# Performance work log

Measured on AMD Instinct MI355X. Metric: run time of the kernel, lower is better.

## Reference

```python
import jax, jax.numpy as jnp
import numpy as np

TEMPERATURE = 0.2
EPS = 1e-10

def setup_inputs() -> dict:
    key = jax.random.key(0)
    x = jax.random.normal(key, (8, 1024, 64, 64), dtype=jnp.float32)
    return {"x": x}

def reference(x):
    B, C, H, W = x.shape
    xf = x.reshape(B, C, H * W)                      # [B, C, HW]
    dot = jnp.einsum('bcn,bdn->bcd', xf, xf) / TEMPERATURE  # [B, C, C]
    logits = jax.nn.softmax(dot, axis=-1)
    diag = jnp.diagonal(logits, axis1=-2, axis2=-1)  # [B, C]
    loss = -jnp.log(diag + EPS)
    return jnp.mean(loss)
```

## Files before the change

### kernel.cpp

```cpp
#include <hip/hip_runtime.h>
#include <hip/hip_bf16.h>

#define BATCH 8
#define CCH 1024
#define NHW 4096
#define SCALE 5.0f
#define ROWS (BATCH * CCH)

typedef unsigned char u8;
typedef unsigned int u32;
typedef __attribute__((ext_vector_type(4))) float float4v;
typedef __attribute__((ext_vector_type(4))) u32 uint4v;

#define VMW(N) asm volatile("s_waitcnt vmcnt(" #N ")" ::: "memory")

__device__ __forceinline__ void async_load16(const void* gsrc, void* ldst) {
    __builtin_amdgcn_global_load_lds(
        (__attribute__((address_space(1))) void*)gsrc,
        (__attribute__((address_space(3))) void*)ldst,
        16, 0, 0);
}

__device__ __forceinline__ u32 pk4_fp8(float a, float b, float c, float d) {
    u32 v = __builtin_amdgcn_cvt_pk_fp8_f32(a, b, 0, false);
    v = __builtin_amdgcn_cvt_pk_fp8_f32(c, d, v, true);
    return v;
}

__device__ __forceinline__ float ssq4_fp8(u32 q) {
    float d0 = __builtin_amdgcn_cvt_f32_fp8(q, 0);
    float d1 = __builtin_amdgcn_cvt_f32_fp8(q, 1);
    float d2 = __builtin_amdgcn_cvt_f32_fp8(q, 2);
    float d3 = __builtin_amdgcn_cvt_f32_fp8(q, 3);
    return d0 * d0 + d1 * d1 + d2 * d2 + d3 * d3;
}

template <bool CONVERT>
__global__ __launch_bounds__(256) void prep_kernel(const float* __restrict__ x,
                                                   u8* __restrict__ xq,
                                                   float* __restrict__ diag,
                                                   float* __restrict__ l_acc,
                                                   u32* __restrict__ counter) {
    const int row = blockIdx.x;
    const int tid = threadIdx.x;
    const float* src = x + (size_t)row * NHW;
    float ssum = 0.f;
#pragma unroll
    for (int p = 0; p < 4; ++p) {
        const int idx = p * 1024 + tid * 4;
        float4 v = *(const float4*)(src + idx);
        const u32 q = pk4_fp8(v.x, v.y, v.z, v.w);
        ssum += ssq4_fp8(q);
        if (CONVERT) *(u32*)(xq + (size_t)row * NHW + idx) = q;
    }
#pragma unroll
    for (int m = 1; m < 64; m <<= 1) ssum += __shfl_xor(ssum, m);
    __shared__ float red[4];
    if ((tid & 63) == 0) red[tid >> 6] = ssum;
    __syncthreads();
    if (tid == 0) {
        diag[row] = (red[0] + red[1] + red[2] + red[3]) * SCALE;
        l_acc[row] = 0.f;
        if (row == 0) *counter = 0;
    }
}

template <bool QSRC>
__global__ __launch_bounds__(256) void gram_kernel(const u8* __restrict__ Xq,
                                                   const float* __restrict__ Xf,
                                                   const float* __restrict__ diag,
                                                   float* __restrict__ l_acc,
                                                   float* __restrict__ num,
                                                   u32* __restrict__ counter,
                                                   float* __restrict__ out) {
    __shared__ __align__(16) u8 As[2][16384];
    __shared__ __align__(16) u8 Bs[2][8192];

    const int bid = blockIdx.x;
    const int b = bid & 7;
    const int t = bid >> 3;

    int bi = 0;
#pragma unroll
    for (int i = 7; i >= 1; --i) {
        if (t >= i * (17 - i)) { bi = i; break; }
    }
    const int bj2 = 2 * bi + (t - bi * (17 - bi));
    const bool aliasB = (bj2 == 2 * bi) || (bj2 == 2 * bi + 1);

    const int tid  = threadIdx.x;
    const int lane = tid & 63;
    const int w    = tid >> 6;
    const int wm   = w >> 1;
    const int wn   = w & 1;

    const int st_r  = lane >> 3;
    const int st_kc = (lane & 7) ^ st_r;

    const u8*    pA  = nullptr; const u8*    pB  = nullptr;
    const float* pAf = nullptr; const float* pBf = nullptr;
    if (QSRC) {
        const u8* baseX = Xq + (size_t)b * CCH * NHW;
        pA = baseX + (size_t)(bi * 128 + w * 32 + st_r) * NHW + st_kc * 16;
        pB = baseX + (size_t)(bj2 * 64 + w * 16 + st_r) * NHW + st_kc * 16;
    } else {
        const float* baseXf = Xf + (size_t)b * CCH * NHW;
        pAf = baseXf + (size_t)(bi * 128 + w * 32 + st_r) * NHW + st_kc * 16;
        pBf = baseXf + (size_t)(bj2 * 64 + w * 16 + st_r) * NHW + st_kc * 16;
    }

    float4v acc[4][2] = {};

    auto stage = [&](int buf, int K0) {
        if (QSRC) {
#pragma unroll
            for (int t8 = 0; t8 < 4; ++t8)
                async_load16(pA + (size_t)(t8 * 8) * NHW + K0,
                             As[buf] + (size_t)(w * 32 + t8 * 8) * 128);
            if (!aliasB) {
#pragma unroll
                for (int t8 = 0; t8 < 2; ++t8)
                    async_load16(pB + (size_t)(t8 * 8) * NHW + K0,
                                 Bs[buf] + (size_t)(w * 16 + t8 * 8) * 128);
            }
        } else {
#pragma unroll
            for (int t8 = 0; t8 < 4; ++t8) {
                const float* s = pAf + (size_t)(t8 * 8) * NHW + K0;
                float4 f0 = *(const float4*)(s);
                float4 f1 = *(const float4*)(s + 4);
                float4 f2 = *(const float4*)(s + 8);
                float4 f3 = *(const float4*)(s + 12);
                uint4v d;
                d.x = pk4_fp8(f0.x, f0.y, f0.z, f0.w);
                d.y = pk4_fp8(f1.x, f1.y, f1.z, f1.w);
                d.z = pk4_fp8(f2.x, f2.y, f2.z, f2.w);
                d.w = pk4_fp8(f3.x, f3.y, f3.z, f3.w);
                *(uint4v*)(As[buf] + (size_t)(w * 32 + t8 * 8 + st_r) * 128 + (lane & 7) * 16) = d;
            }
            if (!aliasB) {
#pragma unroll
                for (int t8 = 0; t8 < 2; ++t8) {
                    const float* s = pBf + (size_t)(t8 * 8) * NHW + K0;
                    float4 f0 = *(const float4*)(s);
                    float4 f1 = *(const float4*)(s + 4);
                    float4 f2 = *(const float4*)(s + 8);
                    float4 f3 = *(const float4*)(s + 12);
                    uint4v d;
                    d.x = pk4_fp8(f0.x, f0.y, f0.z, f0.w);
                    d.y = pk4_fp8(f1.x, f1.y, f1.z, f1.w);
                    d.z = pk4_fp8(f2.x, f2.y, f2.z, f2.w);
                    d.w = pk4_fp8(f3.x, f3.y, f3.z, f3.w);
                    *(uint4v*)(Bs[buf] + (size_t)(w * 16 + t8 * 8 + st_r) * 128 + (lane & 7) * 16) = d;
                }
            }
        }
    };

    stage(0, 0);
    if (!QSRC) __syncthreads();

    const int q  = lane >> 4;
    const int rl = lane & 15;

    for (int i = 0; i < NHW / 128; ++i) {
        const int cur = i & 1;
        const int K0n = (i + 1) * 128;
        const bool more = (K0n < NHW);
        if (more) stage(cur ^ 1, K0n);

        if (QSRC) {
            if (more) {
                if (aliasB) VMW(4); else VMW(6);
            } else {
                VMW(0);
            }
            __builtin_amdgcn_s_barrier();
            __builtin_amdgcn_sched_barrier(0);
        } else {
            __syncthreads();
        }

        const u8* Ab = As[cur];
        const u8* Bb = aliasB ? (Ab + (size_t)(bj2 - 2 * bi) * 64 * 128) : Bs[cur];
#pragma unroll
        for (int s = 0; s < 4; ++s) {
            const int cbase = 2 * s + (q >> 1);
            const int boff  = (int)((cbase ^ (rl & 7)) * 16 + (q & 1) * 8);
            long af[4], bf[2];
#pragma unroll
            for (int mt = 0; mt < 4; ++mt)
                af[mt] = *(const long*)(Ab + (size_t)(wm * 64 + mt * 16 + rl) * 128 + boff);
#pragma unroll
            for (int nt = 0; nt < 2; ++nt)
                bf[nt] = *(const long*)(Bb + (size_t)(wn * 32 + nt * 16 + rl) * 128 + boff);
#pragma unroll
            for (int mt = 0; mt < 4; ++mt)
#pragma unroll
                for (int nt = 0; nt < 2; ++nt)
                    acc[mt][nt] = __builtin_amdgcn_mfma_f32_16x16x32_fp8_fp8(af[mt], bf[nt], acc[mt][nt], 0, 0, 0);
        }

        if (QSRC) {
            __builtin_amdgcn_sched_barrier(0);
            __builtin_amdgcn_s_barrier();
        } else {
            __syncthreads();
        }
    }

    const int cl = lane & 15;
    const int rowbase = bi * 128 + wm * 64;
    const int colbase = bj2 * 64 + wn * 32;
    const float* dgb = diag + b * CCH;
    float* lb = l_acc + b * CCH;

#pragma unroll
    for (int mt = 0; mt < 4; ++mt) {
#pragma unroll
        for (int reg = 0; reg < 4; ++reg) {
            const int gr = rowbase + mt * 16 + q * 4 + reg;
            const float dg = dgb[gr];
            float s = 0.f;
#pragma unroll
            for (int nt = 0; nt < 2; ++nt) {
                const int gc = colbase + nt * 16 + cl;
                const float e = __expf(acc[mt][nt][reg] * SCALE - dg);
                if (gr <= gc) s += e;
                if (gr == gc) num[b * CCH + gr] = e;
            }
            s += __shfl_xor(s, 1);
            s += __shfl_xor(s, 2);
            s += __shfl_xor(s, 4);
            s += __shfl_xor(s, 8);
            if (cl == 0) atomicAdd(lb + gr, s);
        }
    }

#pragma unroll
    for (int nt = 0; nt < 2; ++nt) {
        const int gc = colbase + nt * 16 + cl;
        const float dgc = dgb[gc];
        float s = 0.f;
#pragma unroll
        for (int mt = 0; mt < 4; ++mt) {
#pragma unroll
            for (int reg = 0; reg < 4; ++reg) {
                const int gr = rowbase + mt * 16 + q * 4 + reg;
                if (gr < gc) s += __expf(acc[mt][nt][reg] * SCALE - dgc);
            }
        }
        s += __shfl_xor(s, 16);
        s += __shfl_xor(s, 32);
        if (lane < 16) atomicAdd(lb + gc, s);
    }

    __shared__ u32 lastflag;
    __threadfence();
    __syncthreads();
    if (tid == 0) {
        const u32 old = atomicAdd(counter, 1);
        lastflag = (old == (u32)(gridDim.x - 1)) ? 1u : 0u;
    }
    __syncthreads();
    if (lastflag) {
        __threadfence();
        float s = 0.f;
        for (int r = tid; r < ROWS; r += 256) {
            const float d = num[r] / l_acc[r];
            s += -__logf(d + 1e-10f);
        }
#pragma unroll
        for (int m = 1; m < 64; m <<= 1) s += __shfl_xor(s, m);
        __shared__ float red[4];
        if ((tid & 63) == 0) red[tid >> 6] = s;
        __syncthreads();
        if (tid == 0)
            out[0] = (red[0] + red[1] + red[2] + red[3]) * (1.0f / (float)ROWS);
    }
}

extern "C" void kernel_launch(void* const* d_in, const int* in_sizes, int n_in,
                              void* d_out, int out_size, void* d_ws, size_t ws_size,
                              hipStream_t stream) {
    const float* x = (const float*)d_in[0];
    float* out = (float*)d_out;

    const size_t xq_bytes   = (size_t)BATCH * CCH * NHW;
    const size_t stat_bytes = (size_t)ROWS * 4;
    const bool fast = ws_size >= xq_bytes + 3 * stat_bytes + 64;

    const int ntiles = 72;

    if (fast) {
        u8*    xq      = (u8*)d_ws;
        float* diag    = (float*)((char*)d_ws + xq_bytes);
        float* l_acc   = diag + ROWS;
        float* num     = l_acc + ROWS;
        u32*   counter = (u32*)(num + ROWS);
        prep_kernel<true><<<ROWS, 256, 0, stream>>>(x, xq, diag, l_acc, counter);
        gram_kernel<true><<<BATCH * ntiles, 256, 0, stream>>>(xq, nullptr, diag, l_acc, num, counter, out);
    } else {
        float* diag    = (float*)d_ws;
        float* l_acc   = diag + ROWS;
        float* num     = l_acc + ROWS;
        u32*   counter = (u32*)(num + ROWS);
        prep_kernel<false><<<ROWS, 256, 0, stream>>>(x, nullptr, diag, l_acc, counter);
        gram_kernel<false><<<BATCH * ntiles, 256, 0, stream>>>(nullptr, x, diag, l_acc, num, counter, out);
    }
}
```

Baseline: 277.1 us.

## Shrink Gram tiles to 64x64 upper-triangular and simplify pipeline barriers

The symmetric Gram product is now tiled into 64x64 blocks over the upper triangle, giving 136 tiles per batch instead of 72 tiles of 128x64. This cuts redundant area, halves the A-tile LDS footprint and gives more, smaller blocks for better occupancy and wave balance across CUs. The hand-tuned vmcnt waits and split s_barriers are replaced with plain __syncthreads, which simplifies the double-buffered pipeline. In exchange, each MFMA needs more global and LDS traffic, and the prefetch overlap may weaken because all outstanding loads are drained every iteration.

```diff
diff --git a/kernel.cpp b/kernel.cpp
--- a/kernel.cpp
+++ b/kernel.cpp
@@ -11,8 +11,6 @@
 typedef unsigned int u32;
 typedef __attribute__((ext_vector_type(4))) float float4v;
 typedef __attribute__((ext_vector_type(4))) u32 uint4v;
-
-#define VMW(N) asm volatile("s_waitcnt vmcnt(" #N ")" ::: "memory")
 
 __device__ __forceinline__ void async_load16(const void* gsrc, void* ldst) {
     __builtin_amdgcn_global_load_lds(
@@ -73,7 +71,7 @@
                                                    float* __restrict__ num,
                                                    u32* __restrict__ counter,
                                                    float* __restrict__ out) {
-    __shared__ __align__(16) u8 As[2][16384];
+    __shared__ __align__(16) u8 As[2][8192];
     __shared__ __align__(16) u8 Bs[2][8192];
 
     const int bid = blockIdx.x;
@@ -82,11 +80,11 @@
 
     int bi = 0;
 #pragma unroll
-    for (int i = 7; i >= 1; --i) {
-        if (t >= i * (17 - i)) { bi = i; break; }
-    }
-    const int bj2 = 2 * bi + (t - bi * (17 - bi));
-    const bool aliasB = (bj2 == 2 * bi) || (bj2 == 2 * bi + 1);
+    for (int i = 15; i >= 1; --i) {
+        if (t >= (i * (33 - i)) / 2) { bi = i; break; }
+    }
+    const int bj = bi + (t - (bi * (33 - bi)) / 2);
+    const bool aliasB = (bj == bi);
 
     const int tid  = threadIdx.x;
     const int lane = tid & 63;
@@ -101,22 +99,22 @@
     const float* pAf = nullptr; const float* pBf = nullptr;
     if (QSRC) {
         const u8* baseX = Xq + (size_t)b * CCH * NHW;
-        pA = baseX + (size_t)(bi * 128 + w * 32 + st_r) * NHW + st_kc * 16;
-        pB = baseX + (size_t)(bj2 * 64 + w * 16 + st_r) * NHW + st_kc * 16;
+        pA = baseX + (size_t)(bi * 64 + w * 16 + st_r) * NHW + st_kc * 16;
+        pB = baseX + (size_t)(bj * 64 + w * 16 + st_r) * NHW + st_kc * 16;
     } else {
         const float* baseXf = Xf + (size_t)b * CCH * NHW;
-        pAf = baseXf + (size_t)(bi * 128 + w * 32 + st_r) * NHW + st_kc * 16;
-        pBf = baseXf + (size_t)(bj2 * 64 + w * 16 + st_r) * NHW + st_kc * 16;
-    }
-
-    float4v acc[4][2] = {};
+        pAf = baseXf + (size_t)(bi * 64 + w * 16 + st_r) * NHW + st_kc * 16;
+        pBf = baseXf + (size_t)(bj * 64 + w * 16 + st_r) * NHW + st_kc * 16;
+    }
+
+    float4v acc[2][2] = {};
 
     auto stage = [&](int buf, int K0) {
         if (QSRC) {
 #pragma unroll
-            for (int t8 = 0; t8 < 4; ++t8)
+            for (int t8 = 0; t8 < 2; ++t8)
                 async_load16(pA + (size_t)(t8 * 8) * NHW + K0,
-                             As[buf] + (size_t)(w * 32 + t8 * 8) * 128);
+                             As[buf] + (size_t)(w * 16 + t8 * 8) * 128);
             if (!aliasB) {
 #pragma unroll
                 for (int t8 = 0; t8 < 2; ++t8)
@@ -125,7 +123,7 @@
             }
         } else {
 #pragma unroll
-            for (int t8 = 0; t8 < 4; ++t8) {
+            for (int t8 = 0; t8 < 2; ++t8) {
                 const float* s = pAf + (size_t)(t8 * 8) * NHW + K0;
                 float4 f0 = *(const float4*)(s);
                 float4 f1 = *(const float4*)(s + 4);
@@ -136,7 +134,7 @@
                 d.y = pk4_fp8(f1.x, f1.y, f1.z, f1.w);
                 d.z = pk4_fp8(f2.x, f2.y, f2.z, f2.w);
                 d.w = pk4_fp8(f3.x, f3.y, f3.z, f3.w);
-                *(uint4v*)(As[buf] + (size_t)(w * 32 + t8 * 8 + st_r) * 128 + (lane & 7) * 16) = d;
+                *(uint4v*)(As[buf] + (size_t)(w * 16 + t8 * 8 + st_r) * 128 + (lane & 7) * 16) = d;
             }
             if (!aliasB) {
 #pragma unroll
@@ -158,7 +156,7 @@
     };
 
     stage(0, 0);
-    if (!QSRC) __syncthreads();
+    __syncthreads();
 
     const int q  = lane >> 4;
     const int rl = lane & 15;
@@ -166,57 +164,38 @@
     for (int i = 0; i < NHW / 128; ++i) {
         const int cur = i & 1;
         const int K0n = (i + 1) * 128;
-        const bool more = (K0n < NHW);
-        if (more) stage(cur ^ 1, K0n);
-
-        if (QSRC) {
-            if (more) {
-                if (aliasB) VMW(4); else VMW(6);
-            } else {
-                VMW(0);
-            }
-            __builtin_amdgcn_s_barrier();
-            __builtin_amdgcn_sched_barrier(0);
-        } else {
-            __syncthreads();
-        }
+        if (K0n < NHW) stage(cur ^ 1, K0n);
 
         const u8* Ab = As[cur];
-        const u8* Bb = aliasB ? (Ab + (size_t)(bj2 - 2 * bi) * 64 * 128) : Bs[cur];
+        const u8* Bb = aliasB ? Ab : Bs[cur];
 #pragma unroll
         for (int s = 0; s < 4; ++s) {
             const int cbase = 2 * s + (q >> 1);
             const int boff  = (int)((cbase ^ (rl & 7)) * 16 + (q & 1) * 8);
-            long af[4], bf[2];
-#pragma unroll
-            for (int mt = 0; mt < 4; ++mt)
-                af[mt] = *(const long*)(Ab + (size_t)(wm * 64 + mt * 16 + rl) * 128 + boff);
+            long af[2], bf[2];
+#pragma unroll
+            for (int mt = 0; mt < 2; ++mt)
+                af[mt] = *(const long*)(Ab + (size_t)(wm * 32 + mt * 16 + rl) * 128 + boff);
 #pragma unroll
             for (int nt = 0; nt < 2; ++nt)
                 bf[nt] = *(const long*)(Bb + (size_t)(wn * 32 + nt * 16 + rl) * 128 + boff);
 #pragma unroll
-            for (int mt = 0; mt < 4; ++mt)
+            for (int mt = 0; mt < 2; ++mt)
 #pragma unroll
                 for (int nt = 0; nt < 2; ++nt)
                     acc[mt][nt] = __builtin_amdgcn_mfma_f32_16x16x32_fp8_fp8(af[mt], bf[nt], acc[mt][nt], 0, 0, 0);
         }
-
-        if (QSRC) {
-            __builtin_amdgcn_sched_barrier(0);
-            __builtin_amdgcn_s_barrier();
-        } else {
-            __syncthreads();
-        }
+        __syncthreads();
     }
 
     const int cl = lane & 15;
-    const int rowbase = bi * 128 + wm * 64;
-    const int colbase = bj2 * 64 + wn * 32;
+    const int rowbase = bi * 64 + wm * 32;
+    const int colbase = bj * 64 + wn * 32;
     const float* dgb = diag + b * CCH;
     float* lb = l_acc + b * CCH;
 
 #pragma unroll
-    for (int mt = 0; mt < 4; ++mt) {
+    for (int mt = 0; mt < 2; ++mt) {
 #pragma unroll
         for (int reg = 0; reg < 4; ++reg) {
             const int gr = rowbase + mt * 16 + q * 4 + reg;
@@ -243,7 +222,7 @@
         const float dgc = dgb[gc];
         float s = 0.f;
 #pragma unroll
-        for (int mt = 0; mt < 4; ++mt) {
+        for (int mt = 0; mt < 2; ++mt) {
 #pragma unroll
             for (int reg = 0; reg < 4; ++reg) {
                 const int gr = rowbase + mt * 16 + q * 4 + reg;
@@ -290,7 +269,7 @@
     const size_t stat_bytes = (size_t)ROWS * 4;
     const bool fast = ws_size >= xq_bytes + 3 * stat_bytes + 64;
 
-    const int ntiles = 72;
+    const int ntiles = 136;
 
     if (fast) {
         u8*    xq      = (u8*)d_ws;
```

Result: slower. 314.0 us (+13.3%).

## Enlarge Gram tiles to 128x128 upper-triangle blocks and simplify pipeline sync

Applied to the files above, without the earlier changes.

Switches the Gram kernel from 128x64 tiles (72 per batch) to square 128x128 tiles covering the upper triangle (36 per batch). Each wave now computes a 64x64 sub-tile with a 4x4 MFMA accumulator grid, and the B buffer is doubled. This raises data reuse per byte loaded and halves the number of blocks. The hand-tuned vmcnt waits and split s_barrier calls are replaced by a single __syncthreads per iteration, which may weaken overlap between loads and compute. The change also costs more LDS and registers per block, lowering occupancy.

```diff
diff --git a/kernel.cpp b/kernel.cpp
--- a/kernel.cpp
+++ b/kernel.cpp
@@ -11,8 +11,6 @@
 typedef unsigned int u32;
 typedef __attribute__((ext_vector_type(4))) float float4v;
 typedef __attribute__((ext_vector_type(4))) u32 uint4v;
-
-#define VMW(N) asm volatile("s_waitcnt vmcnt(" #N ")" ::: "memory")
 
 __device__ __forceinline__ void async_load16(const void* gsrc, void* ldst) {
     __builtin_amdgcn_global_load_lds(
@@ -74,7 +72,7 @@
                                                    u32* __restrict__ counter,
                                                    float* __restrict__ out) {
     __shared__ __align__(16) u8 As[2][16384];
-    __shared__ __align__(16) u8 Bs[2][8192];
+    __shared__ __align__(16) u8 Bs[2][16384];
 
     const int bid = blockIdx.x;
     const int b = bid & 7;
@@ -83,10 +81,10 @@
     int bi = 0;
 #pragma unroll
     for (int i = 7; i >= 1; --i) {
-        if (t >= i * (17 - i)) { bi = i; break; }
-    }
-    const int bj2 = 2 * bi + (t - bi * (17 - bi));
-    const bool aliasB = (bj2 == 2 * bi) || (bj2 == 2 * bi + 1);
+        if (t >= (i * (17 - i)) / 2) { bi = i; break; }
+    }
+    const int bj = bi + (t - (bi * (17 - bi)) / 2);
+    const bool aliasB = (bj == bi);
 
     const int tid  = threadIdx.x;
     const int lane = tid & 63;
@@ -102,14 +100,14 @@
     if (QSRC) {
         const u8* baseX = Xq + (size_t)b * CCH * NHW;
         pA = baseX + (size_t)(bi * 128 + w * 32 + st_r) * NHW + st_kc * 16;
-        pB = baseX + (size_t)(bj2 * 64 + w * 16 + st_r) * NHW + st_kc * 16;
+        pB = baseX + (size_t)(bj * 128 + w * 32 + st_r) * NHW + st_kc * 16;
     } else {
         const float* baseXf = Xf + (size_t)b * CCH * NHW;
         pAf = baseXf + (size_t)(bi * 128 + w * 32 + st_r) * NHW + st_kc * 16;
-        pBf = baseXf + (size_t)(bj2 * 64 + w * 16 + st_r) * NHW + st_kc * 16;
-    }
-
-    float4v acc[4][2] = {};
+        pBf = baseXf + (size_t)(bj * 128 + w * 32 + st_r) * NHW + st_kc * 16;
+    }
+
+    float4v acc[4][4] = {};
 
     auto stage = [&](int buf, int K0) {
         if (QSRC) {
@@ -119,9 +117,9 @@
                              As[buf] + (size_t)(w * 32 + t8 * 8) * 128);
             if (!aliasB) {
 #pragma unroll
-                for (int t8 = 0; t8 < 2; ++t8)
+                for (int t8 = 0; t8 < 4; ++t8)
                     async_load16(pB + (size_t)(t8 * 8) * NHW + K0,
-                                 Bs[buf] + (size_t)(w * 16 + t8 * 8) * 128);
+                                 Bs[buf] + (size_t)(w * 32 + t8 * 8) * 128);
             }
         } else {
 #pragma unroll
@@ -140,7 +138,7 @@
             }
             if (!aliasB) {
 #pragma unroll
-                for (int t8 = 0; t8 < 2; ++t8) {
+                for (int t8 = 0; t8 < 4; ++t8) {
                     const float* s = pBf + (size_t)(t8 * 8) * NHW + K0;
                     float4 f0 = *(const float4*)(s);
                     float4 f1 = *(const float4*)(s + 4);
@@ -151,14 +149,14 @@
                     d.y = pk4_fp8(f1.x, f1.y, f1.z, f1.w);
                     d.z = pk4_fp8(f2.x, f2.y, f2.z, f2.w);
                     d.w = pk4_fp8(f3.x, f3.y, f3.z, f3.w);
-                    *(uint4v*)(Bs[buf] + (size_t)(w * 16 + t8 * 8 + st_r) * 128 + (lane & 7) * 16) = d;
+                    *(uint4v*)(Bs[buf] + (size_t)(w * 32 + t8 * 8 + st_r) * 128 + (lane & 7) * 16) = d;
                 }
             }
         }
     };
 
     stage(0, 0);
-    if (!QSRC) __syncthreads();
+    __syncthreads();
 
     const int q  = lane >> 4;
     const int rl = lane & 15;
@@ -166,52 +164,33 @@
     for (int i = 0; i < NHW / 128; ++i) {
         const int cur = i & 1;
         const int K0n = (i + 1) * 128;
-        const bool more = (K0n < NHW);
-        if (more) stage(cur ^ 1, K0n);
-
-        if (QSRC) {
-            if (more) {
-                if (aliasB) VMW(4); else VMW(6);
-            } else {
-                VMW(0);
-            }
-            __builtin_amdgcn_s_barrier();
-            __builtin_amdgcn_sched_barrier(0);
-        } else {
-            __syncthreads();
-        }
+        if (K0n < NHW) stage(cur ^ 1, K0n);
 
         const u8* Ab = As[cur];
-        const u8* Bb = aliasB ? (Ab + (size_t)(bj2 - 2 * bi) * 64 * 128) : Bs[cur];
+        const u8* Bb = aliasB ? Ab : Bs[cur];
 #pragma unroll
         for (int s = 0; s < 4; ++s) {
             const int cbase = 2 * s + (q >> 1);
             const int boff  = (int)((cbase ^ (rl & 7)) * 16 + (q & 1) * 8);
-            long af[4], bf[2];
+            long af[4], bf[4];
 #pragma unroll
             for (int mt = 0; mt < 4; ++mt)
                 af[mt] = *(const long*)(Ab + (size_t)(wm * 64 + mt * 16 + rl) * 128 + boff);
 #pragma unroll
-            for (int nt = 0; nt < 2; ++nt)
-                bf[nt] = *(const long*)(Bb + (size_t)(wn * 32 + nt * 16 + rl) * 128 + boff);
+            for (int nt = 0; nt < 4; ++nt)
+                bf[nt] = *(const long*)(Bb + (size_t)(wn * 64 + nt * 16 + rl) * 128 + boff);
 #pragma unroll
             for (int mt = 0; mt < 4; ++mt)
 #pragma unroll
-                for (int nt = 0; nt < 2; ++nt)
+                for (int nt = 0; nt < 4; ++nt)
                     acc[mt][nt] = __builtin_amdgcn_mfma_f32_16x16x32_fp8_fp8(af[mt], bf[nt], acc[mt][nt], 0, 0, 0);
         }
-
-        if (QSRC) {
-            __builtin_amdgcn_sched_barrier(0);
-            __builtin_amdgcn_s_barrier();
-        } else {
-            __syncthreads();
-        }
+        __syncthreads();
     }
 
     const int cl = lane & 15;
     const int rowbase = bi * 128 + wm * 64;
-    const int colbase = bj2 * 64 + wn * 32;
+    const int colbase = bj * 128 + wn * 64;
     const float* dgb = diag + b * CCH;
     float* lb = l_acc + b * CCH;
 
@@ -223,7 +202,7 @@
             const float dg = dgb[gr];
             float s = 0.f;
 #pragma unroll
-            for (int nt = 0; nt < 2; ++nt) {
+            for (int nt = 0; nt < 4; ++nt) {
                 const int gc = colbase + nt * 16 + cl;
                 const float e = __expf(acc[mt][nt][reg] * SCALE - dg);
                 if (gr <= gc) s += e;
@@ -238,7 +217,7 @@
     }
 
 #pragma unroll
-    for (int nt = 0; nt < 2; ++nt) {
+    for (int nt = 0; nt < 4; ++nt) {
         const int gc = colbase + nt * 16 + cl;
         const float dgc = dgb[gc];
         float s = 0.f;
@@ -290,7 +269,7 @@
     const size_t stat_bytes = (size_t)ROWS * 4;
     const bool fast = ws_size >= xq_bytes + 3 * stat_bytes + 64;
 
-    const int ntiles = 72;
+    const int ntiles = 36;
 
     if (fast) {
         u8*    xq      = (u8*)d_ws;
```

Result: faster. 267.5 us (-3.5%).
